# Optimization experiments

Measured on AMD Instinct MI355X. Metric: run time of the kernel, lower is better.

## Reference

```python
import jax, jax.numpy as jnp
import numpy as np

P, F, V = 2048, 8192, 2048


def setup_inputs() -> dict:
    key = jax.random.key(0)
    k1, k2, k3 = jax.random.split(key, 3)
    points = jax.random.normal(k1, (P, 3), dtype=jnp.float32)
    vertices = jax.random.normal(k2, (V, 3), dtype=jnp.float32)
    faces = jax.random.randint(k3, (F, 3), 0, V, dtype=jnp.int32)
    return {"points": points, "vertices": vertices, "faces": faces}


def _triangle_weights(points, a, b, c):
    """Barycentric weights of closest point on each triangle (a,b,c) [F,3]
    for each point [P,3], via Ericson's region classification.
    All pairwise dot products expanded so only [P,F] scalars are materialized
    (never [P,F,3] differences)."""
    ab = b - a  # [F,3]
    ac = c - a  # [F,3]
    pab = points @ ab.T  # [P,F] = dot(p, ab)
    pac = points @ ac.T  # [P,F] = dot(p, ac)
    d1 = pab - jnp.sum(a * ab, -1)  # dot(ab, p-a)
    d2 = pac - jnp.sum(a * ac, -1)  # dot(ac, p-a)
    d3 = pab - jnp.sum(b * ab, -1)  # dot(ab, p-b)
    d4 = pac - jnp.sum(b * ac, -1)  # dot(ac, p-b)
    d5 = pab - jnp.sum(c * ab, -1)  # dot(ab, p-c)
    d6 = pac - jnp.sum(c * ac, -1)  # dot(ac, p-c)
    vc = d1 * d4 - d3 * d2
    vb = d5 * d2 - d1 * d6
    va = d3 * d6 - d5 * d4

    def sdiv(n, d):
        ds = jnp.where(d == 0, 1.0, d)
        return n / ds

    # region 7 (interior) is the default; overwrite with higher-priority
    denom = va + vb + vc
    v7 = sdiv(vb, denom)
    w7 = sdiv(vc, denom)
    w1, w2, w3 = 1.0 - v7 - w7, v7, w7
    # region 6: edge bc
    t6 = sdiv(d4 - d3, (d4 - d3) + (d5 - d6))
    m6 = (va <= 0) & (d4 - d3 >= 0) & (d5 - d6 >= 0)
    w1 = jnp.where(m6, 0.0, w1)
    w2 = jnp.where(m6, 1.0 - t6, w2)
    w3 = jnp.where(m6, t6, w3)
    # region 5: edge ac
    t5 = sdiv(d2, d2 - d6)
    m5 = (vb <= 0) & (d2 >= 0) & (d6 <= 0)
    w1 = jnp.where(m5, 1.0 - t5, w1)
    w2 = jnp.where(m5, 0.0, w2)
    w3 = jnp.where(m5, t5, w3)
    # region 4: vertex c
    m4 = (d6 >= 0) & (d5 <= d6)
    w1 = jnp.where(m4, 0.0, w1)
    w2 = jnp.where(m4, 0.0, w2)
    w3 = jnp.where(m4, 1.0, w3)
    # region 3: edge ab
    t3 = sdiv(d1, d1 - d3)
    m3 = (vc <= 0) & (d1 >= 0) & (d3 <= 0)
    w1 = jnp.where(m3, 1.0 - t3, w1)
    w2 = jnp.where(m3, t3, w2)
    w3 = jnp.where(m3, 0.0, w3)
    # region 2: vertex b
    m2 = (d3 >= 0) & (d4 <= d3)
    w1 = jnp.where(m2, 0.0, w1)
    w2 = jnp.where(m2, 1.0, w2)
    w3 = jnp.where(m2, 0.0, w3)
    # region 1: vertex a
    m1 = (d1 <= 0) & (d2 <= 0)
    w1 = jnp.where(m1, 1.0, w1)
    w2 = jnp.where(m1, 0.0, w2)
    w3 = jnp.where(m1, 0.0, w3)
    return w1, w2, w3  # each [P,F]


def reference(points, vertices, faces):
    # gather per-face vertex triples (the f1/f2/f3 of the torch module)
    a = vertices[faces[:, 0]]  # [F,3]
    b = vertices[faces[:, 1]]
    c = vertices[faces[:, 2]]
    w1, w2, w3 = _triangle_weights(points, a, b, c)  # [P,F] each
    cp = w1[..., None] * a + w2[..., None] * b + w3[..., None] * c  # [P,F,3]
    dist = jnp.sum((points[:, None, :] - cp) ** 2, axis=-1)  # [P,F]
    idx = jnp.argmin(dist, axis=1)  # [P] closest face per point
    gather = lambda w: jnp.take_along_axis(w, idx[:, None], axis=1)[:, 0]
    return idx, gather(w1), gather(w2), gather(w3)
```

## Files before the change

kernel.cpp:

```cpp
#include <hip/hip_runtime.h>
#include <cstdint>

#pragma clang fp contract(off)

#define P_N 2048
#define F_N 8192
#define V_N 2048

#define TPB 256
#define FACES_PER_TILE 32
#define FLOATS_PER_FACE 24

__device__ __forceinline__ void face_setup(
    const float* __restrict__ vertices, const int* __restrict__ faces, int f,
    float* fd)
{
#pragma clang fp contract(off)
    int i0 = faces[3 * f + 0];
    int i1 = faces[3 * f + 1];
    int i2 = faces[3 * f + 2];
    float ax = vertices[3 * i0 + 0], ay = vertices[3 * i0 + 1], az = vertices[3 * i0 + 2];
    float bx = vertices[3 * i1 + 0], by = vertices[3 * i1 + 1], bz = vertices[3 * i1 + 2];
    float cx = vertices[3 * i2 + 0], cy = vertices[3 * i2 + 1], cz = vertices[3 * i2 + 2];
    float abx = bx - ax, aby = by - ay, abz = bz - az;
    float acx = cx - ax, acy = cy - ay, acz = cz - az;
    float daab = (ax * abx + ay * aby) + az * abz;
    float daac = (ax * acx + ay * acy) + az * acz;
    float dbab = (bx * abx + by * aby) + bz * abz;
    float dbac = (bx * acx + by * acy) + bz * acz;
    float dcab = (cx * abx + cy * aby) + cz * abz;
    float dcac = (cx * acx + cy * acy) + cz * acz;
    fd[0] = ax;  fd[1] = ay;  fd[2] = az;
    fd[3] = bx;  fd[4] = by;  fd[5] = bz;
    fd[6] = cx;  fd[7] = cy;  fd[8] = cz;
    fd[9] = abx; fd[10] = aby; fd[11] = abz;
    fd[12] = acx; fd[13] = acy; fd[14] = acz;
    fd[15] = daab; fd[16] = daac; fd[17] = dbab;
    fd[18] = dbac; fd[19] = dcab; fd[20] = dcac;
}

__device__ __forceinline__ void tri_eval_exact(
    float px, float py, float pz,
    const float* fd,
    float& w1o, float& w2o, float& w3o, float& disto)
{
#pragma clang fp contract(off)
    const float ax = fd[0], ay = fd[1], az = fd[2];
    const float bx = fd[3], by = fd[4], bz = fd[5];
    const float cx = fd[6], cy = fd[7], cz = fd[8];
    const float abx = fd[9], aby = fd[10], abz = fd[11];
    const float acx = fd[12], acy = fd[13], acz = fd[14];
    const float daab = fd[15], daac = fd[16], dbab = fd[17];
    const float dbac = fd[18], dcab = fd[19], dcac = fd[20];

    float pab = fmaf(pz, abz, fmaf(py, aby, px * abx));
    float pac = fmaf(pz, acz, fmaf(py, acy, px * acx));

    float d1 = pab - daab;
    float d2 = pac - daac;
    float d3 = pab - dbab;
    float d4 = pac - dbac;
    float d5 = pab - dcab;
    float d6 = pac - dcac;

    float vc = d1 * d4 - d3 * d2;
    float vb = d5 * d2 - d1 * d6;
    float va = d3 * d6 - d5 * d4;

    float denom = (va + vb) + vc;
    float dn = (denom == 0.0f) ? 1.0f : denom;
    float v7 = vb / dn;
    float w7 = vc / dn;
    float w1 = (1.0f - v7) - w7;
    float w2 = v7;
    float w3 = w7;

    float e63 = d4 - d3;
    float e65 = d5 - d6;
    float t6d = e63 + e65; t6d = (t6d == 0.0f) ? 1.0f : t6d;
    float t6 = e63 / t6d;
    if ((va <= 0.0f) & (e63 >= 0.0f) & (e65 >= 0.0f)) { w1 = 0.0f; w2 = 1.0f - t6; w3 = t6; }

    float t5d = d2 - d6; t5d = (t5d == 0.0f) ? 1.0f : t5d;
    float t5 = d2 / t5d;
    if ((vb <= 0.0f) & (d2 >= 0.0f) & (d6 <= 0.0f)) { w1 = 1.0f - t5; w2 = 0.0f; w3 = t5; }

    if ((d6 >= 0.0f) & (d5 <= d6)) { w1 = 0.0f; w2 = 0.0f; w3 = 1.0f; }

    float t3d = d1 - d3; t3d = (t3d == 0.0f) ? 1.0f : t3d;
    float t3 = d1 / t3d;
    if ((vc <= 0.0f) & (d1 >= 0.0f) & (d3 <= 0.0f)) { w1 = 1.0f - t3; w2 = t3; w3 = 0.0f; }

    if ((d3 >= 0.0f) & (d4 <= d3)) { w1 = 0.0f; w2 = 1.0f; w3 = 0.0f; }

    if ((d1 <= 0.0f) & (d2 <= 0.0f)) { w1 = 1.0f; w2 = 0.0f; w3 = 0.0f; }

    float cpx = (w1 * ax + w2 * bx) + w3 * cx;
    float cpy = (w1 * ay + w2 * by) + w3 * cy;
    float cpz = (w1 * az + w2 * bz) + w3 * cz;
    float dx = px - cpx, dy = py - cpy, dz = pz - cpz;
    float dist = (dx * dx + dy * dy) + dz * dz;

    w1o = w1; w2o = w2; w3o = w3; disto = dist;
}

__global__ __launch_bounds__(TPB) void k_scan(
    const float* __restrict__ points,
    const float* __restrict__ vertices,
    const int* __restrict__ faces,
    unsigned long long* __restrict__ best)
{
    __shared__ float sf[FACES_PER_TILE][FLOATS_PER_FACE];

    const int pblk = blockIdx.x;
    const int fblk = blockIdx.y;
    const int t = threadIdx.x;

    if (t < FACES_PER_TILE) {
        int f = fblk * FACES_PER_TILE + t;
        float fd[21];
        face_setup(vertices, faces, f, fd);
#pragma unroll
        for (int k = 0; k < 21; ++k) sf[t][k] = fd[k];
    }
    __syncthreads();

    const int p = pblk * TPB + t;
    const float px = points[3 * p + 0];
    const float py = points[3 * p + 1];
    const float pz = points[3 * p + 2];

    unsigned int bestdb = 0xffffffffu;
    int bestf = 0;
    const int fbase = fblk * FACES_PER_TILE;

#pragma unroll 4
    for (int j = 0; j < FACES_PER_TILE; ++j) {
        float w1, w2, w3, dist;
        tri_eval_exact(px, py, pz, &sf[j][0], w1, w2, w3, dist);
        unsigned int db = __float_as_uint(dist);
        if (dist != dist) db = 0u;
        if (db < bestdb) { bestdb = db; bestf = fbase + j; }
    }

    unsigned long long key =
        ((unsigned long long)bestdb << 32) | (unsigned int)bestf;
    atomicMin(&best[p], key);
}

__global__ __launch_bounds__(TPB) void k_final(
    const float* __restrict__ points,
    const float* __restrict__ vertices,
    const int* __restrict__ faces,
    const unsigned long long* __restrict__ best,
    float* __restrict__ out)
{
    const int p = blockIdx.x * TPB + threadIdx.x;
    if (p >= P_N) return;
    unsigned long long bk = best[p];
    int f = (int)(bk & 0xffffffffull);

    float fd[21];
    face_setup(vertices, faces, f, fd);

    const float px = points[3 * p + 0];
    const float py = points[3 * p + 1];
    const float pz = points[3 * p + 2];
    float w1, w2, w3, dist;
    tri_eval_exact(px, py, pz, fd, w1, w2, w3, dist);

    out[p] = (float)f;
    out[P_N + p] = w1;
    out[2 * P_N + p] = w2;
    out[3 * P_N + p] = w3;
}

extern "C" void kernel_launch(void* const* d_in, const int* in_sizes, int n_in,
                              void* d_out, int out_size, void* d_ws, size_t ws_size,
                              hipStream_t stream)
{
    const float* points = (const float*)d_in[0];
    const float* vertices = (const float*)d_in[1];
    const int* faces = (const int*)d_in[2];
    float* out = (float*)d_out;
    unsigned long long* best = (unsigned long long*)d_ws;

    hipMemsetAsync(d_ws, 0xFF, P_N * sizeof(unsigned long long), stream);

    dim3 grid(P_N / TPB, F_N / FACES_PER_TILE);
    k_scan<<<grid, TPB, 0, stream>>>(points, vertices, faces, best);
    k_final<<<(P_N + TPB - 1) / TPB, TPB, 0, stream>>>(points, vertices, faces, best, out);
}
```

Baseline: 68.93 us.

## Pack face pairs into float2 math and collapse region selection to two divisions

Shared face data is transposed to a structure-of-arrays layout so two adjacent faces load as float2 vectors, and the dot products, cross terms and distance are computed with packed two-wide float operations. The per-face region classification now selects a numerator and denominator first, so only two divisions run per face instead of five. The aim is to lower ALU and divide cost in the scan loop, at the price of more select instructions and some register pressure.

```diff
diff --git a/kernel.cpp b/kernel.cpp
--- a/kernel.cpp
+++ b/kernel.cpp
@@ -2,6 +2,8 @@
 #include <cstdint>
 
 #pragma clang fp contract(off)
+
+typedef float v2f __attribute__((ext_vector_type(2)));
 
 #define P_N 2048
 #define F_N 8192
@@ -9,7 +11,6 @@
 
 #define TPB 256
 #define FACES_PER_TILE 32
-#define FLOATS_PER_FACE 24
 
 __device__ __forceinline__ void face_setup(
     const float* __restrict__ vertices, const int* __restrict__ faces, int f,
@@ -39,6 +40,35 @@
     fd[18] = dbac; fd[19] = dcab; fd[20] = dcac;
 }
 
+__device__ __forceinline__ void region_w(
+    float d1, float d2, float d3, float d4, float d5, float d6,
+    float va, float vb, float vc, float e63, float e65, float denom,
+    float& w1, float& w2, float& w3)
+{
+#pragma clang fp contract(off)
+    bool m1 = (d1 <= 0.0f) & (d2 <= 0.0f);
+    bool m2 = (d3 >= 0.0f) & (d4 <= d3);
+    bool m3 = (vc <= 0.0f) & (d1 >= 0.0f) & (d3 <= 0.0f);
+    bool m4 = (d6 >= 0.0f) & (d5 <= d6);
+    bool m5 = (vb <= 0.0f) & (d2 >= 0.0f) & (d6 <= 0.0f);
+    bool m6 = (va <= 0.0f) & (e63 >= 0.0f) & (e65 >= 0.0f);
+    bool anym = m1 | m2 | m3 | m4 | m5 | m6;
+
+    float n1  = m1 ? 0.0f : m2 ? 0.0f : m3 ? d1          : m4 ? 0.0f : m5 ? d2          : m6 ? e63         : vb;
+    float ds1 = m1 ? 1.0f : m2 ? 1.0f : m3 ? (d1 - d3)   : m4 ? 1.0f : m5 ? (d2 - d6)   : m6 ? (e63 + e65) : denom;
+    ds1 = (ds1 == 0.0f) ? 1.0f : ds1;
+    float n2  = anym ? 0.0f : vc;
+    float ds2 = anym ? 1.0f : ((denom == 0.0f) ? 1.0f : denom);
+
+    float q1 = n1 / ds1;
+    float q2 = n2 / ds2;
+    float u = (1.0f - q1) - q2;
+
+    w1 = m1 ? 1.0f : m2 ? 0.0f : m3 ? u    : m4 ? 0.0f : m5 ? u    : m6 ? 0.0f : u;
+    w2 = m1 ? 0.0f : m2 ? 1.0f : m3 ? q1   : m4 ? 0.0f : m5 ? 0.0f : m6 ? u    : q1;
+    w3 = m1 ? 0.0f : m2 ? 0.0f : m3 ? 0.0f : m4 ? 1.0f : m5 ? q1   : m6 ? q1   : q2;
+}
+
 __device__ __forceinline__ void tri_eval_exact(
     float px, float py, float pz,
     const float* fd,
@@ -110,7 +140,8 @@
     const int* __restrict__ faces,
     unsigned long long* __restrict__ best)
 {
-    __shared__ float sf[FACES_PER_TILE][FLOATS_PER_FACE];
+#pragma clang fp contract(off)
+    __shared__ float sq[21][FACES_PER_TILE];
 
     const int pblk = blockIdx.x;
     const int fblk = blockIdx.y;
@@ -121,7 +152,7 @@
         float fd[21];
         face_setup(vertices, faces, f, fd);
 #pragma unroll
-        for (int k = 0; k < 21; ++k) sf[t][k] = fd[k];
+        for (int k = 0; k < 21; ++k) sq[k][t] = fd[k];
     }
     __syncthreads();
 
@@ -129,18 +160,70 @@
     const float px = points[3 * p + 0];
     const float py = points[3 * p + 1];
     const float pz = points[3 * p + 2];
+    const v2f pxv = {px, px};
+    const v2f pyv = {py, py};
+    const v2f pzv = {pz, pz};
 
     unsigned int bestdb = 0xffffffffu;
     int bestf = 0;
     const int fbase = fblk * FACES_PER_TILE;
 
-#pragma unroll 4
-    for (int j = 0; j < FACES_PER_TILE; ++j) {
-        float w1, w2, w3, dist;
-        tri_eval_exact(px, py, pz, &sf[j][0], w1, w2, w3, dist);
-        unsigned int db = __float_as_uint(dist);
-        if (dist != dist) db = 0u;
-        if (db < bestdb) { bestdb = db; bestf = fbase + j; }
+#pragma unroll 2
+    for (int j = 0; j < FACES_PER_TILE; j += 2) {
+#define LD2(q) (*(const v2f*)&sq[q][j])
+        v2f axv = LD2(0),  ayv = LD2(1),  azv = LD2(2);
+        v2f bxv = LD2(3),  byv = LD2(4),  bzv = LD2(5);
+        v2f cxv = LD2(6),  cyv = LD2(7),  czv = LD2(8);
+        v2f abxv = LD2(9),  abyv = LD2(10), abzv = LD2(11);
+        v2f acxv = LD2(12), acyv = LD2(13), aczv = LD2(14);
+        v2f daabv = LD2(15), daacv = LD2(16), dbabv = LD2(17);
+        v2f dbacv = LD2(18), dcabv = LD2(19), dcacv = LD2(20);
+#undef LD2
+
+        v2f pab = __builtin_elementwise_fma(pzv, abzv,
+                    __builtin_elementwise_fma(pyv, abyv, pxv * abxv));
+        v2f pac = __builtin_elementwise_fma(pzv, aczv,
+                    __builtin_elementwise_fma(pyv, acyv, pxv * acxv));
+
+        v2f d1 = pab - daabv;
+        v2f d2 = pac - daacv;
+        v2f d3 = pab - dbabv;
+        v2f d4 = pac - dbacv;
+        v2f d5 = pab - dcabv;
+        v2f d6 = pac - dcacv;
+
+        v2f vcv = d1 * d4 - d3 * d2;
+        v2f vbv = d5 * d2 - d1 * d6;
+        v2f vav = d3 * d6 - d5 * d4;
+
+        v2f e63 = d4 - d3;
+        v2f e65 = d5 - d6;
+        v2f denom = (vav + vbv) + vcv;
+
+        float w1a, w2a, w3a, w1b, w2b, w3b;
+        region_w(d1.x, d2.x, d3.x, d4.x, d5.x, d6.x,
+                 vav.x, vbv.x, vcv.x, e63.x, e65.x, denom.x, w1a, w2a, w3a);
+        region_w(d1.y, d2.y, d3.y, d4.y, d5.y, d6.y,
+                 vav.y, vbv.y, vcv.y, e63.y, e65.y, denom.y, w1b, w2b, w3b);
+
+        v2f w1v = {w1a, w1b};
+        v2f w2v = {w2a, w2b};
+        v2f w3v = {w3a, w3b};
+
+        v2f cpx = (w1v * axv + w2v * bxv) + w3v * cxv;
+        v2f cpy = (w1v * ayv + w2v * byv) + w3v * cyv;
+        v2f cpz = (w1v * azv + w2v * bzv) + w3v * czv;
+        v2f dx = pxv - cpx, dy = pyv - cpy, dz = pzv - cpz;
+        v2f dist = (dx * dx + dy * dy) + dz * dz;
+
+        float da = dist.x;
+        float db = dist.y;
+        unsigned int ua = __float_as_uint(da);
+        unsigned int ub = __float_as_uint(db);
+        if (da != da) ua = 0u;
+        if (db != db) ub = 0u;
+        if (ua < bestdb) { bestdb = ua; bestf = fbase + j; }
+        if (ub < bestdb) { bestdb = ub; bestf = fbase + j + 1; }
     }
 
     unsigned long long key =
```

Result: faster. 55.95 us (-18.8%).
